# Kernel optimization log

Measured on AMD Instinct MI355X. Metric: run time of the kernel, lower is better.

Reference implementation:

```python
import jax, jax.numpy as jnp
import numpy as np

EMBED = 768
HEAD = 64
SEQ = 4096
BATCH = 4


def setup_inputs() -> dict:
    key = jax.random.key(0)
    ks = jax.random.split(key, 7)
    s = 1.0 / np.sqrt(EMBED)
    x = jax.random.normal(ks[0], (BATCH, SEQ, EMBED), dtype=jnp.float32)
    Wq = jax.random.uniform(ks[1], (EMBED, HEAD), jnp.float32, -s, s)
    bq = jax.random.uniform(ks[2], (HEAD,), jnp.float32, -s, s)
    Wk = jax.random.uniform(ks[3], (EMBED, HEAD), jnp.float32, -s, s)
    bk = jax.random.uniform(ks[4], (HEAD,), jnp.float32, -s, s)
    Wv = jax.random.uniform(ks[5], (EMBED, HEAD), jnp.float32, -s, s)
    bv = jax.random.uniform(ks[6], (HEAD,), jnp.float32, -s, s)
    return {"x": x, "Wq": Wq, "bq": bq, "Wk": Wk, "bk": bk, "Wv": Wv, "bv": bv}


def reference(x, Wq, bq, Wk, bk, Wv, bv):
    # x: [B,T,E]
    Q = x @ Wq + bq  # [B,T,H]
    K = x @ Wk + bk
    V = x @ Wv + bv
    scale = 1.0 / jnp.sqrt(jnp.asarray(HEAD, dtype=x.dtype))
    wei = jnp.einsum('bqh,bkh->bqk', Q, K) * scale  # [B,T,T]
    T = x.shape[1]
    causal = jnp.tril(jnp.ones((T, T), dtype=bool))
    wei = jnp.where(causal, wei, -jnp.inf)
    wei = jax.nn.softmax(wei, axis=-1)
    return jnp.einsum('bqk,bkh->bqh', wei, V)  # [B,T,H]
```

## Files before the change

### kernel.cpp

```cpp
#include <hip/hip_runtime.h>


#define BB 4
#define TT 4096
#define EE 768
#define HH 64
#define BT (BB*TT)

typedef __attribute__((ext_vector_type(8))) short short8;
typedef __attribute__((ext_vector_type(4))) float f32x4;
#define MFMA16(a,b,c) __builtin_amdgcn_mfma_f32_16x16x32_bf16(a,b,c,0,0,0)
#define QSCALE 0.18033688011112042f

static __device__ __forceinline__ float bflo(unsigned a){ return __uint_as_float(a << 16); }
static __device__ __forceinline__ unsigned short f2bf(float f){
    unsigned x = __float_as_uint(f);
    x += 0x7fffu + ((x >> 16) & 1u);
    return (unsigned short)(x >> 16);
}
template<int FP32>
static __device__ __forceinline__ float ldin(const void* p, int idx){
    if (FP32) return ((const float*)p)[idx];
    return bflo(((const unsigned short*)p)[idx]);
}

template<int FP32>
static __device__ void wt_body(const void* W, int wi, int e0, unsigned short* wt){
    __shared__ unsigned short ts[64 * 72];
    const int tid = threadIdx.x;
    #pragma unroll
    for (int p = 0; p < 2; p++){
        int i = p * 256 + tid;
        int r = i >> 3, g = i & 7;
        unsigned short v[8];
        if (FP32){
            const float* src = (const float*)W + (size_t)(e0 + r) * HH + g * 8;
            const float4 a = *(const float4*)src, b = *(const float4*)(src + 4);
            v[0]=f2bf(a.x); v[1]=f2bf(a.y); v[2]=f2bf(a.z); v[3]=f2bf(a.w);
            v[4]=f2bf(b.x); v[5]=f2bf(b.y); v[6]=f2bf(b.z); v[7]=f2bf(b.w);
        } else {
            const unsigned short* src = (const unsigned short*)W + (size_t)(e0 + r) * HH + g * 8;
            #pragma unroll
            for (int j = 0; j < 8; j++) v[j] = src[j];
        }
        #pragma unroll
        for (int j = 0; j < 8; j++) ts[r * 72 + g * 8 + j] = v[j];
    }
    __syncthreads();
    #pragma unroll
    for (int p = 0; p < 2; p++){
        int i = p * 256 + tid;
        int h = i >> 3, g = i & 7;
        unsigned short v[8];
        #pragma unroll
        for (int j = 0; j < 8; j++) v[j] = ts[(g * 8 + j) * 72 + h];
        unsigned short* dst = wt + (size_t)(wi * 64 + h) * EE + e0 + g * 8;
        uint4 pk;
        pk.x = (unsigned)v[0] | ((unsigned)v[1] << 16);
        pk.y = (unsigned)v[2] | ((unsigned)v[3] << 16);
        pk.z = (unsigned)v[4] | ((unsigned)v[5] << 16);
        pk.w = (unsigned)v[6] | ((unsigned)v[7] << 16);
        *(uint4*)dst = pk;
    }
}
__global__ __launch_bounds__(256) void wt_kernel(
    const unsigned short* xu, const void* Wq, const void* Wk, const void* Wv,
    unsigned short* wt, int* flag){
    __shared__ int cnt;
    const int tid = threadIdx.x;
    if (tid == 0) cnt = 0;
    __syncthreads();
    int c = 0;
    #pragma unroll
    for (int i = 0; i < 16; i++){
        unsigned u = xu[tid * 16 + i];
        unsigned e = (u >> 7) & 0xFFu;
        if (e >= 140u) c++;
    }
    atomicAdd(&cnt, c);
    __syncthreads();
    const int fp32 = (cnt > 32) ? 1 : 0;
    if (blockIdx.x == 0 && tid == 0) *flag = fp32;
    const int wi = blockIdx.x / 12;
    const int e0 = (blockIdx.x % 12) * 64;
    const void* W = (wi == 0) ? Wq : (wi == 1) ? Wk : Wv;
    if (fp32) wt_body<1>(W, wi, e0, wt);
    else      wt_body<0>(W, wi, e0, wt);
}

template<int FP32>
static __device__ void qkv_body(const void* x, const unsigned short* wt,
    const void* bq, const void* bk, const void* bv,
    unsigned short* Qw, unsigned short* Kw, unsigned short* VTw,
    unsigned short* xs, unsigned short* wsl)
{
    const int tid = threadIdx.x, lane = tid & 63, w = tid >> 6;
    const int l15 = lane & 15, quad = lane >> 4;
    const int z = blockIdx.x;
    const int m0 = (z >> 1) * 32;
    const int nh = z & 1;
    const int rh = (w & 1) * 16;
    const int ngl = (w >> 1) * 3;

    f32x4 acc[3];
    #pragma unroll
    for (int i = 0; i < 3; i++) acc[i] = (f32x4)(0.f);

    const int srow = tid >> 3, sg = tid & 7;

    const float*          xsF = (const float*)x + (size_t)(m0 + srow) * EE + sg * 8;
    const unsigned short* xsB = (const unsigned short*)x + (size_t)(m0 + srow) * EE + sg * 8;
    const unsigned short* ws0 = wt + (size_t)(nh * 96 + srow) * EE + sg * 8;
    const unsigned short* ws1 = ws0 + (size_t)32 * EE;
    const unsigned short* ws2 = ws0 + (size_t)64 * EE;

    float4 xa, xb;
    short8 xv;
    short8 wr0, wr1, wr2;

    if (FP32){ xa = *(const float4*)xsF; xb = *(const float4*)(xsF + 4); }
    else     { xv = *(const short8*)xsB; }
    wr0 = *(const short8*)ws0;
    wr1 = *(const short8*)ws1;
    wr2 = *(const short8*)ws2;

    for (int c = 0; c < 12; c++){
        __syncthreads();
        {
            short8 v;
            if (FP32){
                v[0]=(short)f2bf(xa.x); v[1]=(short)f2bf(xa.y); v[2]=(short)f2bf(xa.z); v[3]=(short)f2bf(xa.w);
                v[4]=(short)f2bf(xb.x); v[5]=(short)f2bf(xb.y); v[6]=(short)f2bf(xb.z); v[7]=(short)f2bf(xb.w);
            } else {
                v = xv;
            }
            *(short8*)&xs[srow * 72 + sg * 8] = v;
        }
        *(short8*)&wsl[(     srow) * 72 + sg * 8] = wr0;
        *(short8*)&wsl[(32 + srow) * 72 + sg * 8] = wr1;
        *(short8*)&wsl[(64 + srow) * 72 + sg * 8] = wr2;
        if (c < 11){
            const int c1 = (c + 1) * 64;
            if (FP32){ xa = *(const float4*)(xsF + c1); xb = *(const float4*)(xsF + c1 + 4); }
            else     { xv = *(const short8*)(xsB + c1); }
            wr0 = *(const short8*)(ws0 + c1);
            wr1 = *(const short8*)(ws1 + c1);
            wr2 = *(const short8*)(ws2 + c1);
        }
        __syncthreads();
        #pragma unroll
        for (int kst = 0; kst < 2; kst++){
            const short8 a = *(const short8*)&xs[(rh + l15) * 72 + kst * 32 + quad * 8];
            #pragma unroll
            for (int nf = 0; nf < 3; nf++){
                const short8 bfr = *(const short8*)&wsl[((ngl + nf) * 16 + l15) * 72 + kst * 32 + quad * 8];
                acc[nf] = MFMA16(a, bfr, acc[nf]);
            }
        }
    }
    #pragma unroll
    for (int nf = 0; nf < 3; nf++){
        const int gi = nh * 6 + ngl + nf;
        const int wi = gi >> 2;
        const int h = (gi & 3) * 16 + l15;
        const void* bp = (wi == 0) ? bq : (wi == 1) ? bk : bv;
        const float bias = ldin<FP32>(bp, h);
        if (wi == 0){
            #pragma unroll
            for (int rr = 0; rr < 4; rr++){
                const int tok = m0 + rh + quad * 4 + rr;
                Qw[(size_t)tok * HH + h] = f2bf((acc[nf][rr] + bias) * QSCALE);
            }
        } else if (wi == 1){
            #pragma unroll
            for (int rr = 0; rr < 4; rr++){
                const int tok = m0 + rh + quad * 4 + rr;
                Kw[(size_t)tok * HH + h] = f2bf(acc[nf][rr] + bias);
            }
        } else {
            const int tok0 = m0 + rh + quad * 4;
            const int bloc = tok0 >> 12;
            const int tl = tok0 & 4095;
            uint2 pk;
            pk.x = (unsigned)f2bf(acc[nf][0] + bias) | ((unsigned)f2bf(acc[nf][1] + bias) << 16);
            pk.y = (unsigned)f2bf(acc[nf][2] + bias) | ((unsigned)f2bf(acc[nf][3] + bias) << 16);
            *(uint2*)&VTw[(size_t)(bloc * 64 + h) * TT + tl] = pk;
        }
    }
}
__global__ __launch_bounds__(256, 2) void qkv_kernel(
    const void* x, const unsigned short* wt,
    const void* bq, const void* bk, const void* bv,
    unsigned short* Qw, unsigned short* Kw, unsigned short* VTw, const int* flag){
    __shared__ unsigned short xs[32 * 72];
    __shared__ unsigned short wsl[96 * 72];
    if (*flag) qkv_body<1>(x, wt, bq, bk, bv, Qw, Kw, VTw, xs, wsl);
    else       qkv_body<0>(x, wt, bq, bk, bv, Qw, Kw, VTw, xs, wsl);
}

__global__ __launch_bounds__(512, 2) void attn_kernel(
    const unsigned short* __restrict__ Q,
    const unsigned short* __restrict__ K, const unsigned short* __restrict__ VT,
    void* __restrict__ out, const int* __restrict__ flag)
{
    __shared__ unsigned short sbuf[8][2304];
    __shared__ float lpart[8][32];

    const int mode = *flag;
    const int z = blockIdx.x;
    const int b = z & 3;
    const int qt = 127 - (z >> 2);
    const int q0 = qt * 32;
    const int nkb = (qt >> 1) + 1;
    const int tid = threadIdx.x;
    const int lane = tid & 63;
    const int w = tid >> 6;
    const int l15 = lane & 15, quad = lane >> 4;
    const int brow = b * TT;

    f32x4 O[2][4];
    float lsum[2][4];
    #pragma unroll
    for (int mt = 0; mt < 2; mt++)
        #pragma unroll
        for (int i = 0; i < 4; i++){ O[mt][i] = (f32x4)(0.f); lsum[mt][i] = 0.f; }

    if (w < nkb){
        short8 qf[2][2];
        #pragma unroll
        for (int mt = 0; mt < 2; mt++)
            #pragma unroll
            for (int kst = 0; kst < 2; kst++)
                qf[mt][kst] = *(const short8*)(Q + (size_t)(brow + q0 + mt * 16 + l15) * HH + kst * 32 + quad * 8);

        short8 kf[4][2];
        #pragma unroll
        for (int c = 0; c < 4; c++)
            #pragma unroll
            for (int kst = 0; kst < 2; kst++)
                kf[c][kst] = *(const short8*)(K + (size_t)(brow + w * 64 + c * 16 + l15) * HH + kst * 32 + quad * 8);

        for (int u = w; u < nkb; u += 8){
            const int k0 = u * 64;
            f32x4 sacc[2][4];
            #pragma unroll
            for (int mt = 0; mt < 2; mt++)
                #pragma unroll
                for (int c = 0; c < 4; c++){
                    sacc[mt][c] = (f32x4)(0.f);
                    sacc[mt][c] = MFMA16(qf[mt][0], kf[c][0], sacc[mt][c]);
                    sacc[mt][c] = MFMA16(qf[mt][1], kf[c][1], sacc[mt][c]);
                }
            short8 vf[4][2];
            #pragma unroll
            for (int c = 0; c < 4; c++)
                #pragma unroll
                for (int kst = 0; kst < 2; kst++)
                    vf[c][kst] = *(const short8*)(VT + (size_t)(b * 64 + c * 16 + l15) * TT + k0 + kst * 32 + quad * 8);
            if (u + 8 < nkb){
                const int kn0 = (u + 8) * 64;
                #pragma unroll
                for (int c = 0; c < 4; c++)
                    #pragma unroll
                    for (int kst = 0; kst < 2; kst++)
                        kf[c][kst] = *(const short8*)(K + (size_t)(brow + kn0 + c * 16 + l15) * HH + kst * 32 + quad * 8);
            }
            const bool diag = (u == nkb - 1);
            #pragma unroll
            for (int mt = 0; mt < 2; mt++){
                #pragma unroll
                for (int c = 0; c < 4; c++){
                    #pragma unroll
                    for (int rr = 0; rr < 4; rr++){
                        float sv = sacc[mt][c][rr];
                        if (diag){
                            const int kg = k0 + c * 16 + l15;
                            const int qg = q0 + mt * 16 + quad * 4 + rr;
                            sv = (kg <= qg) ? sv : -1e30f;
                        }
                        const float p = exp2f(sv);
                        lsum[mt][rr] += p;
                        sbuf[w][mt * 1152 + (quad * 4 + rr) * 72 + c * 16 + l15] =
                            (unsigned short)(__float_as_uint(p) >> 16);
                    }
                }
            }
            #pragma unroll
            for (int mt = 0; mt < 2; mt++){
                const short8 pf0 = *(const short8*)&sbuf[w][mt * 1152 + l15 * 72 + quad * 8];
                const short8 pf1 = *(const short8*)&sbuf[w][mt * 1152 + l15 * 72 + 32 + quad * 8];
                #pragma unroll
                for (int c2 = 0; c2 < 4; c2++){
                    O[mt][c2] = MFMA16(pf0, vf[c2][0], O[mt][c2]);
                    O[mt][c2] = MFMA16(pf1, vf[c2][1], O[mt][c2]);
                }
            }
        }
        #pragma unroll
        for (int mt = 0; mt < 2; mt++)
            #pragma unroll
            for (int rr = 0; rr < 4; rr++){
                #pragma unroll
                for (int off = 1; off < 16; off <<= 1)
                    lsum[mt][rr] += __shfl_xor(lsum[mt][rr], off, 64);
            }
    }
    #pragma unroll
    for (int mt = 0; mt < 2; mt++)
        #pragma unroll
        for (int rr = 0; rr < 4; rr++){
            const int row = mt * 16 + quad * 4 + rr;
            #pragma unroll
            for (int c2 = 0; c2 < 4; c2++)
                sbuf[w][row * 72 + c2 * 16 + l15] = f2bf(O[mt][c2][rr]);
            if (l15 == 0) lpart[w][row] = lsum[mt][rr];
        }
    __syncthreads();
    #pragma unroll
    for (int i = 0; i < 4; i++){
        const int e = i * 512 + tid;
        const int r = e >> 6, h = e & 63;
        float num = 0.f, den = 0.f;
        #pragma unroll
        for (int ww = 0; ww < 8; ww++){
            num += bflo(sbuf[ww][r * 72 + h]);
            den += lpart[ww][r];
        }
        const float ov = num / den;
        const size_t gi = (size_t)(brow + q0 + r) * HH + h;
        if (mode) ((float*)out)[gi] = ov;
        else      ((unsigned short*)out)[gi] = f2bf(ov);
    }
}

extern "C" void kernel_launch(void* const* d_in, const int* in_sizes, int n_in,
                              void* d_out, int out_size, void* d_ws, size_t ws_size,
                              hipStream_t stream) {
    const void* x  = d_in[0];
    const void* Wq = d_in[1];
    const void* bq = d_in[2];
    const void* Wk = d_in[3];
    const void* bk = d_in[4];
    const void* Wv = d_in[5];
    const void* bv = d_in[6];

    unsigned short* Qw  = (unsigned short*)d_ws;
    unsigned short* Kw  = Qw + (size_t)BT * HH;
    unsigned short* VTw = Kw + (size_t)BT * HH;
    unsigned short* wt  = VTw + (size_t)BT * HH;
    int* flag  = (int*)(wt + (size_t)192 * EE);

    wt_kernel<<<36, 256, 0, stream>>>((const unsigned short*)x, Wq, Wk, Wv, wt, flag);
    qkv_kernel<<<1024, 256, 0, stream>>>(x, wt, bq, bk, bv, Qw, Kw, VTw, flag);
    attn_kernel<<<512, 512, 0, stream>>>(Qw, Kw, VTw, d_out, flag);
}
```

Measured before the change: 150.5 us.

## Software-pipeline QK MFMA ahead of softmax and compute row sums via MFMA

The next block's QK^T MFMAs are issued right after the current block's exp/store to shared memory, and the K prefetch moves one iteration further ahead, so matrix work overlaps the VALU softmax. The per-row probability sum is now accumulated with extra MFMAs against a ones vector instead of scalar adds and a shuffle reduction. The sums now use the bf16-truncated probabilities, matching the values fed to PV. This adds two MFMAs per tile and raises register pressure from keeping sacc live across iterations.

```diff
diff --git a/kernel.cpp b/kernel.cpp
--- a/kernel.cpp
+++ b/kernel.cpp
@@ -198,6 +198,18 @@
     else       qkv_body<0>(x, wt, bq, bk, bv, Qw, Kw, VTw, xs, wsl);
 }
 
+static __device__ __forceinline__ void qk8(
+    const short8 (&qf)[2][2], const short8 (&kf)[4][2], f32x4 (&s)[2][4])
+{
+    #pragma unroll
+    for (int mt = 0; mt < 2; mt++)
+        #pragma unroll
+        for (int c = 0; c < 4; c++){
+            s[mt][c] = (f32x4)(0.f);
+            s[mt][c] = MFMA16(qf[mt][0], kf[c][0], s[mt][c]);
+            s[mt][c] = MFMA16(qf[mt][1], kf[c][1], s[mt][c]);
+        }
+}
 __global__ __launch_bounds__(512, 2) void attn_kernel(
     const unsigned short* __restrict__ Q,
     const unsigned short* __restrict__ K, const unsigned short* __restrict__ VT,
@@ -218,12 +230,16 @@
     const int l15 = lane & 15, quad = lane >> 4;
     const int brow = b * TT;
 
+    const short8 VONES = (short8)(short)0x3F80;
+
     f32x4 O[2][4];
-    float lsum[2][4];
-    #pragma unroll
-    for (int mt = 0; mt < 2; mt++)
-        #pragma unroll
-        for (int i = 0; i < 4; i++){ O[mt][i] = (f32x4)(0.f); lsum[mt][i] = 0.f; }
+    f32x4 Lk[2];
+    #pragma unroll
+    for (int mt = 0; mt < 2; mt++){
+        Lk[mt] = (f32x4)(0.f);
+        #pragma unroll
+        for (int i = 0; i < 4; i++) O[mt][i] = (f32x4)(0.f);
+    }
 
     if (w < nkb){
         short8 qf[2][2];
@@ -240,31 +256,25 @@
             for (int kst = 0; kst < 2; kst++)
                 kf[c][kst] = *(const short8*)(K + (size_t)(brow + w * 64 + c * 16 + l15) * HH + kst * 32 + quad * 8);
 
+        f32x4 sacc[2][4];
+        qk8(qf, kf, sacc);
+        if (w + 8 < nkb){
+            const int kn0 = (w + 8) * 64;
+            #pragma unroll
+            for (int c = 0; c < 4; c++)
+                #pragma unroll
+                for (int kst = 0; kst < 2; kst++)
+                    kf[c][kst] = *(const short8*)(K + (size_t)(brow + kn0 + c * 16 + l15) * HH + kst * 32 + quad * 8);
+        }
+
         for (int u = w; u < nkb; u += 8){
             const int k0 = u * 64;
-            f32x4 sacc[2][4];
-            #pragma unroll
-            for (int mt = 0; mt < 2; mt++)
-                #pragma unroll
-                for (int c = 0; c < 4; c++){
-                    sacc[mt][c] = (f32x4)(0.f);
-                    sacc[mt][c] = MFMA16(qf[mt][0], kf[c][0], sacc[mt][c]);
-                    sacc[mt][c] = MFMA16(qf[mt][1], kf[c][1], sacc[mt][c]);
-                }
             short8 vf[4][2];
             #pragma unroll
             for (int c = 0; c < 4; c++)
                 #pragma unroll
                 for (int kst = 0; kst < 2; kst++)
                     vf[c][kst] = *(const short8*)(VT + (size_t)(b * 64 + c * 16 + l15) * TT + k0 + kst * 32 + quad * 8);
-            if (u + 8 < nkb){
-                const int kn0 = (u + 8) * 64;
-                #pragma unroll
-                for (int c = 0; c < 4; c++)
-                    #pragma unroll
-                    for (int kst = 0; kst < 2; kst++)
-                        kf[c][kst] = *(const short8*)(K + (size_t)(brow + kn0 + c * 16 + l15) * HH + kst * 32 + quad * 8);
-            }
             const bool diag = (u == nkb - 1);
             #pragma unroll
             for (int mt = 0; mt < 2; mt++){
@@ -279,16 +289,28 @@
                             sv = (kg <= qg) ? sv : -1e30f;
                         }
                         const float p = exp2f(sv);
-                        lsum[mt][rr] += p;
                         sbuf[w][mt * 1152 + (quad * 4 + rr) * 72 + c * 16 + l15] =
                             (unsigned short)(__float_as_uint(p) >> 16);
                     }
                 }
             }
+            if (u + 8 < nkb){
+                qk8(qf, kf, sacc);
+                if (u + 16 < nkb){
+                    const int kn0 = (u + 16) * 64;
+                    #pragma unroll
+                    for (int c = 0; c < 4; c++)
+                        #pragma unroll
+                        for (int kst = 0; kst < 2; kst++)
+                            kf[c][kst] = *(const short8*)(K + (size_t)(brow + kn0 + c * 16 + l15) * HH + kst * 32 + quad * 8);
+                }
+            }
             #pragma unroll
             for (int mt = 0; mt < 2; mt++){
                 const short8 pf0 = *(const short8*)&sbuf[w][mt * 1152 + l15 * 72 + quad * 8];
                 const short8 pf1 = *(const short8*)&sbuf[w][mt * 1152 + l15 * 72 + 32 + quad * 8];
+                Lk[mt] = MFMA16(pf0, VONES, Lk[mt]);
+                Lk[mt] = MFMA16(pf1, VONES, Lk[mt]);
                 #pragma unroll
                 for (int c2 = 0; c2 < 4; c2++){
                     O[mt][c2] = MFMA16(pf0, vf[c2][0], O[mt][c2]);
@@ -296,14 +318,6 @@
                 }
             }
         }
-        #pragma unroll
-        for (int mt = 0; mt < 2; mt++)
-            #pragma unroll
-            for (int rr = 0; rr < 4; rr++){
-                #pragma unroll
-                for (int off = 1; off < 16; off <<= 1)
-                    lsum[mt][rr] += __shfl_xor(lsum[mt][rr], off, 64);
-            }
     }
     #pragma unroll
     for (int mt = 0; mt < 2; mt++)
@@ -313,7 +327,7 @@
             #pragma unroll
             for (int c2 = 0; c2 < 4; c2++)
                 sbuf[w][row * 72 + c2 * 16 + l15] = f2bf(O[mt][c2][rr]);
-            if (l15 == 0) lpart[w][row] = lsum[mt][rr];
+            if (l15 == 0) lpart[w][row] = Lk[mt][rr];
         }
     __syncthreads();
     #pragma unroll
```

Result: no change. 150.6 us (+0.1%).
